# Performance work log

Measured on AMD Instinct MI355X. Metric: run time of the kernel, lower is better.

## Reference

```python
import jax, jax.numpy as jnp
import numpy as np

EPS = 1e-6
INV_T = 1.0
STEPS = 4
S = 1  # MD_S
R = 1  # MD_R


def setup_inputs() -> dict:
    key = jax.random.key(0)
    k1, k2 = jax.random.split(key)
    # NMF operates on non-negative data -> uniform [0,1)
    x = jax.random.uniform(k1, (4, 16, 160, 72, 72), dtype=jnp.float32)
    bases = jax.random.uniform(k2, (4 * S, 160 // S, R), dtype=jnp.float32)
    # _build_bases: F.normalize(bases, dim=1) -> L2 normalize over D axis
    bases = bases / jnp.maximum(jnp.linalg.norm(bases, axis=1, keepdims=True), 1e-12)
    return {"x": x, "bases": bases}


def _local_step(xr, bases, coef):
    # xr: [B, D, N], bases: [B, D, R], coef: [B, N, R]
    # multiplicative NMF update for coef
    num_c = jnp.einsum('bdn,bdr->bnr', xr, bases)                     # x^T b
    btb = jnp.einsum('bdr,bds->brs', bases, bases)                    # b^T b  [B,R,R]
    coef = coef * num_c / (jnp.einsum('bnr,brs->bns', coef, btb) + EPS)
    # multiplicative NMF update for bases
    num_b = jnp.einsum('bdn,bnr->bdr', xr, coef)                      # x c
    ctc = jnp.einsum('bnr,bns->brs', coef, coef)                      # c^T c  [B,R,R]
    bases = bases * num_b / (jnp.einsum('bdr,brs->bds', bases, ctc) + EPS)
    return bases, coef


def _compute_coef(xr, bases, coef):
    num_c = jnp.einsum('bdn,bdr->bnr', xr, bases)
    btb = jnp.einsum('bdr,bds->brs', bases, bases)
    return coef * num_c / (jnp.einsum('bnr,brs->bns', coef, btb) + EPS)


def reference(x, bases):
    B, C, T, H, W = x.shape
    D = T // S
    N = C * H * W
    xr = x.reshape(B * S, D, N)  # [4, 160, 82944]

    def local_inference(xr, bases):
        coef = jax.nn.softmax(INV_T * jnp.einsum('bdn,bdr->bnr', xr, bases), axis=-1)
        for _ in range(STEPS):
            bases, coef = _local_step(xr, bases, coef)
        return bases, coef

    # local_inference is @torch.no_grad() in the original
    bases_f, coef = jax.lax.stop_gradient(local_inference(xr, bases))
    coef = _compute_coef(xr, bases_f, coef)
    out = jnp.einsum('bdr,bnr->bdn', bases_f, coef)  # bases @ coef^T
    return out.reshape(B, C, T, H, W)
```

## Files before the change

kernel.cpp:

```cpp
#include <hip/hip_runtime.h>
#include <hip/hip_bf16.h>

#define EPS 1e-6f

constexpr int D  = 160;
constexpr int NN = 82944;
constexpr int B  = 4;

typedef __bf16 bf16x8 __attribute__((ext_vector_type(8)));
typedef __bf16 bf16x4 __attribute__((ext_vector_type(4)));
typedef float  floatx4 __attribute__((ext_vector_type(4)));

constexpr int BK = 64;
constexpr int BKP = BK + 8;
constexpr int SLABS = 4;
constexpr int COLS_PER_BLOCK = BK * SLABS;
constexpr int GRAM_BLOCKS = NN / COLS_PER_BLOCK;

__global__ __launch_bounds__(256, 3)
void gram_kernel(const float* __restrict__ x, float* __restrict__ G)
{
    __shared__ __align__(16) __bf16 xs[D * BKP];

    const int tid = threadIdx.x;
    const int batch = blockIdx.y;
    const int w  = tid >> 6;
    const int l  = tid & 63;
    const int lr = l & 15;
    const int lq = l >> 4;
    const int itile0 = (w & 1) * 5;
    const int jtile0 = (w >> 1) * 5;
    const int srow = tid >> 4;
    const int scol = (tid & 15) * 4;

    const float* xb = x + (size_t)batch * D * NN + (size_t)blockIdx.x * COLS_PER_BLOCK;

    floatx4 acc[5][5] = {};

    for (int s = 0; s < SLABS; ++s) {
        const int n0 = s * BK;
        #pragma unroll
        for (int p = 0; p < 10; ++p) {
            const int d = p * 16 + srow;
            float4 v = *(const float4*)(xb + (size_t)d * NN + n0 + scol);
            bf16x4 h = { (__bf16)v.x, (__bf16)v.y, (__bf16)v.z, (__bf16)v.w };
            *(bf16x4*)&xs[d * BKP + scol] = h;
        }
        __syncthreads();
        #pragma unroll
        for (int k = 0; k < BK / 32; ++k) {
            bf16x8 fa[5], fb[5];
            #pragma unroll
            for (int i = 0; i < 5; ++i) {
                fa[i] = *(const bf16x8*)&xs[((itile0 + i) * 16 + lr) * BKP + k * 32 + lq * 8];
                fb[i] = *(const bf16x8*)&xs[((jtile0 + i) * 16 + lr) * BKP + k * 32 + lq * 8];
            }
            #pragma unroll
            for (int i = 0; i < 5; ++i)
                #pragma unroll
                for (int j = 0; j < 5; ++j)
                    acc[i][j] = __builtin_amdgcn_mfma_f32_16x16x32_bf16(fa[i], fb[j], acc[i][j], 0, 0, 0);
        }
        __syncthreads();
    }

    float* Gb = G + (size_t)batch * D * D;
    #pragma unroll
    for (int i = 0; i < 5; ++i) {
        const int d1base = (itile0 + i) * 16 + lq * 4;
        #pragma unroll
        for (int j = 0; j < 5; ++j) {
            const int d2 = (jtile0 + j) * 16 + lr;
            #pragma unroll
            for (int r = 0; r < 4; ++r)
                atomicAdd(&Gb[(size_t)(d1base + r) * D + d2], acc[i][j][r]);
        }
    }
}

__device__ __forceinline__ float block_reduce_bcast(float v, float* red)
{
    #pragma unroll
    for (int off = 32; off > 0; off >>= 1)
        v += __shfl_xor(v, off, 64);
    const int w = threadIdx.x >> 6;
    if ((threadIdx.x & 63) == 0) red[w] = v;
    __syncthreads();
    float s = red[0] + red[1] + red[2] + red[3];
    __syncthreads();
    return s;
}

__global__ __launch_bounds__(256)
void iter_kernel(const float* __restrict__ bases, const float* __restrict__ G,
                 float* __restrict__ bvec, float* __restrict__ svec)
{
    __shared__ float bs[D];
    __shared__ float red[4];
    const int batch = blockIdx.x;
    const int tid = threadIdx.x;
    const float* Gb = G + (size_t)batch * D * D;

    if (tid < D) bs[tid] = bases[batch * D + tid];
    __syncthreads();

    for (int step = 0; step < 4; ++step) {
        float v = (tid < D) ? bs[tid] * bs[tid] : 0.0f;
        const float btb = block_reduce_bcast(v, red);
        const float gamma = btb + EPS;

        float m = 0.0f;
        if (tid < D) {
            const float* row = Gb + (size_t)tid * D;
            #pragma unroll 8
            for (int j = 0; j < D; j += 4) {
                float4 g4 = *(const float4*)(row + j);
                m += g4.x * bs[j] + g4.y * bs[j + 1] + g4.z * bs[j + 2] + g4.w * bs[j + 3];
            }
        }
        float bm = (tid < D) ? bs[tid] * m : 0.0f;
        const float beta = block_reduce_bcast(bm, red);
        const float ctc = beta / (gamma * gamma);

        __syncthreads();
        if (tid < D) {
            const float bd = bs[tid];
            bs[tid] = bd * (m / gamma) / (bd * ctc + EPS);
        }
        __syncthreads();
    }

    float v = (tid < D) ? bs[tid] * bs[tid] : 0.0f;
    const float btb = block_reduce_bcast(v, red);
    const float inv = 1.0f / (btb + EPS);
    if (tid < D) {
        bvec[batch * D + tid] = bs[tid];
        svec[batch * D + tid] = bs[tid] * inv;
    }
}

__global__ __launch_bounds__(256)
void out_kernel(const float* __restrict__ x, const float* __restrict__ bvec,
                const float* __restrict__ svec, float* __restrict__ out)
{
    __shared__ float bsh[D], ssh[D];
    __shared__ floatx4 part[256];

    const int tid = threadIdx.x;
    const int batch = blockIdx.y;
    const int g = tid >> 5;
    const int lane = tid & 31;
    const size_t base = (size_t)batch * D * NN + (size_t)blockIdx.x * 128 + lane * 4;

    if (tid < D) { bsh[tid] = bvec[batch * D + tid]; ssh[tid] = svec[batch * D + tid]; }
    __syncthreads();

    floatx4 t = {0.f, 0.f, 0.f, 0.f};
    #pragma unroll
    for (int d = g; d < D; d += 8) {
        floatx4 xv = *(const floatx4*)(x + base + (size_t)d * NN);
        const float bd = bsh[d];
        t += xv * bd;
    }
    part[tid] = t;
    __syncthreads();
    if (tid < 32) {
        floatx4 s = part[lane];
        #pragma unroll
        for (int k = 1; k < 8; ++k)
            s += part[k * 32 + lane];
        part[lane] = s;
    }
    __syncthreads();
    t = part[lane];

    #pragma unroll
    for (int d = g; d < D; d += 8) {
        const float sd = ssh[d];
        floatx4 o = t * sd;
        __builtin_nontemporal_store(o, (floatx4*)(out + base + (size_t)d * NN));
    }
}

extern "C" void kernel_launch(void* const* d_in, const int* in_sizes, int n_in,
                              void* d_out, int out_size, void* d_ws, size_t ws_size,
                              hipStream_t stream)
{
    (void)in_sizes; (void)n_in; (void)out_size; (void)ws_size;
    const float* x     = (const float*)d_in[0];
    const float* bases = (const float*)d_in[1];
    float* out = (float*)d_out;

    float* G    = (float*)d_out;
    float* bvec = (float*)d_ws;
    float* svec = bvec + B * D;

    hipMemsetAsync(G, 0, (size_t)B * D * D * sizeof(float), stream);
    gram_kernel<<<dim3(GRAM_BLOCKS, B), 256, 0, stream>>>(x, G);
    iter_kernel<<<dim3(B), 256, 0, stream>>>(bases, G, bvec, svec);
    out_kernel<<<dim3(NN / 128, B), 256, 0, stream>>>(x, bvec, svec, out);
}
```

Before: 517.7 us.

## Prefetch next slab in gram kernel and double columns per out block

In the Gram kernel, the next slab of x is loaded into registers while MFMAs run on the current slab in shared memory. It also doubles the slabs per block, which halves the number of atomic adds to G, and lowers occupancy from 3 to 2 blocks per CU. The output kernel now handles 256 columns per block with two independent accumulators, giving more memory-level parallelism and fewer blocks. Register pressure rises, and the smaller grids may underfill the GPU.

```diff
diff --git a/kernel.cpp b/kernel.cpp
--- a/kernel.cpp
+++ b/kernel.cpp
@@ -13,11 +13,11 @@
 
 constexpr int BK = 64;
 constexpr int BKP = BK + 8;
-constexpr int SLABS = 4;
+constexpr int SLABS = 8;
 constexpr int COLS_PER_BLOCK = BK * SLABS;
 constexpr int GRAM_BLOCKS = NN / COLS_PER_BLOCK;
 
-__global__ __launch_bounds__(256, 3)
+__global__ __launch_bounds__(256, 2)
 void gram_kernel(const float* __restrict__ x, float* __restrict__ G)
 {
     __shared__ __align__(16) __bf16 xs[D * BKP];
@@ -34,19 +34,29 @@
     const int scol = (tid & 15) * 4;
 
     const float* xb = x + (size_t)batch * D * NN + (size_t)blockIdx.x * COLS_PER_BLOCK;
+    const float* pbase = xb + (size_t)srow * NN + scol;
 
     floatx4 acc[5][5] = {};
+    float4 pf[10];
+
+    #pragma unroll
+    for (int p = 0; p < 10; ++p)
+        pf[p] = *(const float4*)(pbase + (size_t)p * 16 * NN);
 
     for (int s = 0; s < SLABS; ++s) {
-        const int n0 = s * BK;
+        __syncthreads();
         #pragma unroll
         for (int p = 0; p < 10; ++p) {
-            const int d = p * 16 + srow;
-            float4 v = *(const float4*)(xb + (size_t)d * NN + n0 + scol);
-            bf16x4 h = { (__bf16)v.x, (__bf16)v.y, (__bf16)v.z, (__bf16)v.w };
-            *(bf16x4*)&xs[d * BKP + scol] = h;
-        }
-        __syncthreads();
+            bf16x4 h = { (__bf16)pf[p].x, (__bf16)pf[p].y, (__bf16)pf[p].z, (__bf16)pf[p].w };
+            *(bf16x4*)&xs[(srow + p * 16) * BKP + scol] = h;
+        }
+        __syncthreads();
+        if (s + 1 < SLABS) {
+            const float* pn = pbase + (s + 1) * BK;
+            #pragma unroll
+            for (int p = 0; p < 10; ++p)
+                pf[p] = *(const float4*)(pn + (size_t)p * 16 * NN);
+        }
         #pragma unroll
         for (int k = 0; k < BK / 32; ++k) {
             bf16x8 fa[5], fb[5];
@@ -61,7 +71,6 @@
                 for (int j = 0; j < 5; ++j)
                     acc[i][j] = __builtin_amdgcn_mfma_f32_16x16x32_bf16(fa[i], fb[j], acc[i][j], 0, 0, 0);
         }
-        __syncthreads();
     }
 
     float* Gb = G + (size_t)batch * D * D;
@@ -144,41 +153,54 @@
                 const float* __restrict__ svec, float* __restrict__ out)
 {
     __shared__ float bsh[D], ssh[D];
-    __shared__ floatx4 part[256];
+    __shared__ floatx4 partA[256];
+    __shared__ floatx4 partB[256];
 
     const int tid = threadIdx.x;
     const int batch = blockIdx.y;
     const int g = tid >> 5;
     const int lane = tid & 31;
-    const size_t base = (size_t)batch * D * NN + (size_t)blockIdx.x * 128 + lane * 4;
+    const size_t base0 = (size_t)batch * D * NN + (size_t)blockIdx.x * 256 + lane * 4;
+    const size_t base1 = base0 + 128;
 
     if (tid < D) { bsh[tid] = bvec[batch * D + tid]; ssh[tid] = svec[batch * D + tid]; }
     __syncthreads();
 
-    floatx4 t = {0.f, 0.f, 0.f, 0.f};
+    floatx4 t0 = {0.f, 0.f, 0.f, 0.f};
+    floatx4 t1 = {0.f, 0.f, 0.f, 0.f};
     #pragma unroll
     for (int d = g; d < D; d += 8) {
-        floatx4 xv = *(const floatx4*)(x + base + (size_t)d * NN);
+        floatx4 xv0 = *(const floatx4*)(x + base0 + (size_t)d * NN);
+        floatx4 xv1 = *(const floatx4*)(x + base1 + (size_t)d * NN);
         const float bd = bsh[d];
-        t += xv * bd;
-    }
-    part[tid] = t;
+        t0 += xv0 * bd;
+        t1 += xv1 * bd;
+    }
+    partA[tid] = t0;
+    partB[tid] = t1;
     __syncthreads();
     if (tid < 32) {
-        floatx4 s = part[lane];
-        #pragma unroll
-        for (int k = 1; k < 8; ++k)
-            s += part[k * 32 + lane];
-        part[lane] = s;
-    }
-    __syncthreads();
-    t = part[lane];
+        floatx4 s = partA[tid];
+        #pragma unroll
+        for (int k = 1; k < 8; ++k) s += partA[k * 32 + tid];
+        partA[tid] = s;
+    } else if (tid < 64) {
+        floatx4 s = partB[tid - 32];
+        #pragma unroll
+        for (int k = 1; k < 8; ++k) s += partB[k * 32 + (tid - 32)];
+        partB[tid - 32] = s;
+    }
+    __syncthreads();
+    t0 = partA[lane];
+    t1 = partB[lane];
 
     #pragma unroll
     for (int d = g; d < D; d += 8) {
         const float sd = ssh[d];
-        floatx4 o = t * sd;
-        __builtin_nontemporal_store(o, (floatx4*)(out + base + (size_t)d * NN));
+        floatx4 o0 = t0 * sd;
+        floatx4 o1 = t1 * sd;
+        __builtin_nontemporal_store(o0, (floatx4*)(out + base0 + (size_t)d * NN));
+        __builtin_nontemporal_store(o1, (floatx4*)(out + base1 + (size_t)d * NN));
     }
 }
 
@@ -198,5 +220,5 @@
     hipMemsetAsync(G, 0, (size_t)B * D * D * sizeof(float), stream);
     gram_kernel<<<dim3(GRAM_BLOCKS, B), 256, 0, stream>>>(x, G);
     iter_kernel<<<dim3(B), 256, 0, stream>>>(bases, G, bvec, svec);
-    out_kernel<<<dim3(NN / 128, B), 256, 0, stream>>>(x, bvec, svec, out);
-}
+    out_kernel<<<dim3(NN / 256, B), 256, 0, stream>>>(x, bvec, svec, out);
+}
```

Result: faster. 448.9 us (-13.3%).
